# Kernel optimization log

Hardware: AMD Instinct MI355X
Metric: run time of the kernel (lower is better)

Reference implementation:

```python
import jax, jax.numpy as jnp
import numpy as np

N_E = 1024
E_DIM = 64
BETA = 0.25
DECAY = 0.99
EPSILON = 1e-5


def setup_inputs() -> dict:
    key = jax.random.key(0)
    k1, k2, k3 = jax.random.split(key, 3)
    z = jax.random.normal(k1, (32, E_DIM, 32, 32), dtype=jnp.float32)
    # codebook initialized uniform(-1/n_e, 1/n_e) as in the torch module
    emb_w = jax.random.uniform(k2, (N_E, E_DIM), minval=-1.0 / N_E, maxval=1.0 / N_E, dtype=jnp.float32)
    ema_cluster_size = jnp.ones((N_E,), dtype=jnp.float32)
    ema_w = jax.random.uniform(k3, (N_E, E_DIM), minval=-1.0 / N_E, maxval=1.0 / N_E, dtype=jnp.float32)
    return {"z": z, "emb_w": emb_w, "ema_cluster_size": ema_cluster_size, "ema_w": ema_w}


def reference(z, emb_w, ema_cluster_size, ema_w):
    B, C, H, W = z.shape  # C == E_DIM
    zf = jnp.transpose(z, (0, 2, 3, 1)).reshape(-1, E_DIM)  # [N, e_dim]
    N = zf.shape[0]

    # squared-distance via ||z||^2 + ||e||^2 - 2 z.e (same expansion as torch code)
    d = (jnp.sum(zf * zf, axis=1, keepdims=True)
         + jnp.sum(emb_w * emb_w, axis=1)
         - 2.0 * zf @ emb_w.T)  # [N, n_e]
    idx = jnp.argmin(d, axis=1)  # [N]

    min_encodings = jax.nn.one_hot(idx, N_E, dtype=jnp.float32)  # [N, n_e]
    # cluster stats via scatter-add (equivalent to one-hot matmuls, cheaper)
    cluster_size = jax.ops.segment_sum(jnp.ones((N,), jnp.float32), idx, num_segments=N_E)
    sum_encodings = jax.ops.segment_sum(zf, idx, num_segments=N_E)  # [n_e, e_dim]

    # EMA update (training path, done before the z_q lookup as in torch)
    new_cs = DECAY * ema_cluster_size + (1.0 - DECAY) * cluster_size
    new_w = DECAY * ema_w + (1.0 - DECAY) * sum_encodings
    n = jnp.sum(new_cs)
    cs_norm = (new_cs + EPSILON) / (n + N_E * EPSILON) * n
    new_emb = new_w / cs_norm[:, None]  # updated codebook

    z_q = new_emb[idx].reshape(B, H, W, C).transpose(0, 3, 1, 2)  # [B,C,H,W]
    loss = BETA * jnp.mean((jax.lax.stop_gradient(z_q) - z) ** 2)
    z_q_st = z + jax.lax.stop_gradient(z_q - z)  # straight-through

    avg_probs = cluster_size / N
    perplexity = jnp.exp(-jnp.sum(avg_probs * jnp.log(avg_probs + 1e-10)))
    return loss, z_q_st, perplexity, min_encodings, idx
```

## Files before the change

### kernel.cpp

```cpp
#include <hip/hip_runtime.h>
#include <math.h>

#define NVEC 32768
#define NE   1024
#define ED   64
#define TOT  2097152
#define NCHUNK 8
#define CHUNK  128
#define MT     64

#define O_LOSS   0
#define O_ZQ     1
#define O_PERP   2097153
#define O_MINENC 2097154
#define O_IDX    35651586

#define W_PDIST  0
#define W_PIDX   262144
#define W_CS     524288
#define W_SUMENC 525312
#define W_NEWEMB 590848
#define W_LOSSP  656384

__global__ void __launch_bounds__(256, 3) k_dist(const float* __restrict__ z,
                                                 const float* __restrict__ emb,
                                                 float* __restrict__ pdist,
                                                 int* __restrict__ pidx) {
    __shared__ __align__(16) float s_a[64 * 64];
    __shared__ __align__(16) float s_b[64 * 132];
    __shared__ float s_esq[CHUNK];
    __shared__ float s_zsq[MT];

    int tid = threadIdx.x;
    int k0 = blockIdx.y * CHUNK;
    int n0 = blockIdx.x * MT;
    int b = n0 >> 10, hw0 = n0 & 1023;
    const float* zb = z + b * 65536 + hw0;

#pragma unroll
    for (int j = 0; j < 4; ++j) {
        int f4i = j * 256 + tid;
        int c = f4i >> 4, pos = (f4i & 15) * 4;
        float4 v = *(const float4*)(zb + (c << 10) + pos);
        v.x = __fmul_rn(2.0f, v.x);
        v.y = __fmul_rn(2.0f, v.y);
        v.z = __fmul_rn(2.0f, v.z);
        v.w = __fmul_rn(2.0f, v.w);
        *(float4*)(s_a + c * 64 + pos) = v;
    }
#pragma unroll
    for (int j = 0; j < 8; ++j) {
        int f4i = j * 256 + tid;
        int kl = f4i >> 4, c0 = (f4i & 15) * 4;
        float4 v = *(const float4*)(emb + (size_t)(k0 + kl) * ED + c0);
        s_b[(c0 + 0) * 132 + kl] = v.x;
        s_b[(c0 + 1) * 132 + kl] = v.y;
        s_b[(c0 + 2) * 132 + kl] = v.z;
        s_b[(c0 + 3) * 132 + kl] = v.w;
    }
    __syncthreads();

    if (tid < 128) {
        float r[8];
#pragma unroll
        for (int j = 0; j < 8; ++j) {
            float v = s_b[j * 132 + tid];
            r[j] = __fmul_rn(v, v);
        }
#pragma unroll
        for (int i = 8; i < 64; i += 8)
#pragma unroll
            for (int j = 0; j < 8; ++j) {
                float v = s_b[(i + j) * 132 + tid];
                r[j] = __fadd_rn(r[j], __fmul_rn(v, v));
            }
        s_esq[tid] = __fadd_rn(
            __fadd_rn(__fadd_rn(r[0], r[1]), __fadd_rn(r[2], r[3])),
            __fadd_rn(__fadd_rn(r[4], r[5]), __fadd_rn(r[6], r[7])));
    } else if (tid < 192) {
        int m = tid - 128;
        float r[8];
#pragma unroll
        for (int j = 0; j < 8; ++j) {
            float v = s_a[j * 64 + m];
            r[j] = __fmul_rn(v, v);
        }
#pragma unroll
        for (int i = 8; i < 64; i += 8)
#pragma unroll
            for (int j = 0; j < 8; ++j) {
                float v = s_a[(i + j) * 64 + m];
                r[j] = __fadd_rn(r[j], __fmul_rn(v, v));
            }
        s_zsq[m] = __fmul_rn(0.25f, __fadd_rn(
            __fadd_rn(__fadd_rn(r[0], r[1]), __fadd_rn(r[2], r[3])),
            __fadd_rn(__fadd_rn(r[4], r[5]), __fadd_rn(r[6], r[7]))));
    }
    __syncthreads();

    int mi = tid & 15, ki = tid >> 4;
    int mbase = mi * 4, kbase = ki * 8;

    float acc[4][8];
#pragma unroll
    for (int mu = 0; mu < 4; ++mu)
#pragma unroll
        for (int ku = 0; ku < 8; ++ku) acc[mu][ku] = 0.f;

#pragma unroll 4
    for (int c = 0; c < 64; ++c) {
        float4 av = *(const float4*)(s_a + c * 64 + mbase);
        float4 b0 = *(const float4*)(s_b + c * 132 + kbase);
        float4 b1 = *(const float4*)(s_b + c * 132 + kbase + 4);
        const float* bv = &b0.x;
#pragma unroll
        for (int mu = 0; mu < 4; ++mu) {
            float a = (&av.x)[mu];
            acc[mu][0] = __fmaf_rn(a, b0.x, acc[mu][0]);
            acc[mu][1] = __fmaf_rn(a, b0.y, acc[mu][1]);
            acc[mu][2] = __fmaf_rn(a, b0.z, acc[mu][2]);
            acc[mu][3] = __fmaf_rn(a, b0.w, acc[mu][3]);
            acc[mu][4] = __fmaf_rn(a, b1.x, acc[mu][4]);
            acc[mu][5] = __fmaf_rn(a, b1.y, acc[mu][5]);
            acc[mu][6] = __fmaf_rn(a, b1.z, acc[mu][6]);
            acc[mu][7] = __fmaf_rn(a, b1.w, acc[mu][7]);
        }
        (void)bv;
    }

    float zs[4], es[8];
#pragma unroll
    for (int mu = 0; mu < 4; ++mu) zs[mu] = s_zsq[mbase + mu];
#pragma unroll
    for (int ku = 0; ku < 8; ++ku) es[ku] = s_esq[kbase + ku];

    float bd[4];
    int bix[4];
#pragma unroll
    for (int mu = 0; mu < 4; ++mu) {
        float best = 3.4e38f;
        int bi = k0 + kbase;
#pragma unroll
        for (int ku = 0; ku < 8; ++ku) {
            float d = __fsub_rn(__fadd_rn(zs[mu], es[ku]), acc[mu][ku]);
            if (d < best) { best = d; bi = k0 + kbase + ku; }
        }
        bd[mu] = best;
        bix[mu] = bi;
    }

    __syncthreads();
    float* red_d = s_a;
    int* red_i = (int*)(s_a + 1024);
#pragma unroll
    for (int mu = 0; mu < 4; ++mu) {
        red_d[ki * 64 + mbase + mu] = bd[mu];
        red_i[ki * 64 + mbase + mu] = bix[mu];
    }
    __syncthreads();
    if (tid < MT) {
        float best = red_d[tid];
        int bi = red_i[tid];
#pragma unroll
        for (int q = 1; q < 16; ++q) {
            float d = red_d[q * 64 + tid];
            int i = red_i[q * 64 + tid];
            if (d < best) { best = d; bi = i; }
        }
        pdist[blockIdx.y * NVEC + n0 + tid] = best;
        pidx[blockIdx.y * NVEC + n0 + tid] = bi;
    }
}

__global__ void __launch_bounds__(256) k_combine(const float* __restrict__ pdist,
                                                 int* __restrict__ pidx,
                                                 float* __restrict__ out) {
    __shared__ int sbi[64];
    int n0 = blockIdx.x * 64;
    if (threadIdx.x < 64) {
        int n = n0 + threadIdx.x;
        float best = pdist[n];
        int bi = pidx[n];
#pragma unroll
        for (int q = 1; q < NCHUNK; ++q) {
            float d = pdist[q * NVEC + n];
            int i = pidx[q * NVEC + n];
            if (d < best) { best = d; bi = i; }
        }
        pidx[n] = bi;
        out[O_IDX + n] = (float)bi;
        sbi[threadIdx.x] = bi;
    }
    __syncthreads();
    int wave = threadIdx.x >> 6, lane = threadIdx.x & 63;
    size_t base = (size_t)O_MINENC + (size_t)n0 * NE;
    for (int r = wave; r < 64; r += 4) {
        int rbi = sbi[r];
        float* rp = out + base + (size_t)r * NE;
#pragma unroll
        for (int s = 0; s < 8; ++s) {
            int col = s * 128 + lane * 2;
            float2 v;
            v.x = (col == rbi) ? 1.0f : 0.0f;
            v.y = (col + 1 == rbi) ? 1.0f : 0.0f;
            *(float2*)(rp + col) = v;
        }
    }
}

__global__ void __launch_bounds__(256) k_sumenc(const int* __restrict__ idx,
                                                const float* __restrict__ z,
                                                float* __restrict__ cs,
                                                float* __restrict__ sumenc) {
    int k = blockIdx.x;
    int wave = threadIdx.x >> 6, lane = threadIdx.x & 63;
    float acc = 0.f;
    int cnt = 0;
    int base = wave * 8192;
    for (int it = 0; it < 128; ++it) {
        int n0 = base + it * 64;
        int idv = idx[n0 + lane];
        unsigned long long m = __ballot(idv == k);
        cnt += __popcll(m);
        while (m) {
            int bit = __ffsll((unsigned long long)m) - 1;
            m &= m - 1;
            int n = n0 + bit;
            int b = n >> 10, hw = n & 1023;
            acc = __fadd_rn(acc, z[b * 65536 + lane * 1024 + hw]);
        }
    }
    __shared__ float sacc[4][64];
    __shared__ int scnt[4];
    sacc[wave][lane] = acc;
    if (lane == 0) scnt[wave] = cnt;
    __syncthreads();
    if (wave == 0) {
        float t = __fadd_rn(__fadd_rn(sacc[0][lane], sacc[1][lane]),
                            __fadd_rn(sacc[2][lane], sacc[3][lane]));
        sumenc[k * ED + lane] = t;
        if (lane == 0) cs[k] = (float)(scnt[0] + scnt[1] + scnt[2] + scnt[3]);
    }
}

__global__ void __launch_bounds__(1024) k_ema(const float* __restrict__ ema_cs,
                                              const float* __restrict__ ema_w,
                                              const float* __restrict__ cs,
                                              const float* __restrict__ sumenc,
                                              float* __restrict__ newemb,
                                              float* __restrict__ out) {
    int k = threadIdx.x;
    float c = cs[k];
    float ncs = 0.99f * ema_cs[k] + (1.0f - 0.99f) * c;
    float p = c * (1.0f / (float)NVEC);
    float e = p * logf(p + 1e-10f);
    float rn_ = ncs, re_ = e;
#pragma unroll
    for (int o = 32; o > 0; o >>= 1) {
        rn_ += __shfl_down(rn_, o, 64);
        re_ += __shfl_down(re_, o, 64);
    }
    __shared__ float sn[16], se_[16];
    __shared__ float s_n;
    int wave = k >> 6, lane = k & 63;
    if (lane == 0) { sn[wave] = rn_; se_[wave] = re_; }
    __syncthreads();
    if (k == 0) {
        float tn = 0.f, te = 0.f;
#pragma unroll
        for (int w = 0; w < 16; ++w) { tn += sn[w]; te += se_[w]; }
        s_n = tn;
        out[O_PERP] = expf(-te);
    }
    __syncthreads();
    float nt = s_n;
    float csn = (ncs + 1e-5f) / (nt + 1024.0f * 1e-5f) * nt;
    __shared__ float s_csn[NE];
    s_csn[k] = csn;
    __syncthreads();
    for (int t = k; t < NE * ED; t += 1024) {
        float nw = 0.99f * ema_w[t] + (1.0f - 0.99f) * sumenc[t];
        newemb[t] = nw / s_csn[t >> 6];
    }
}

__global__ void __launch_bounds__(256) k_zq(const float* __restrict__ z,
                                            const int* __restrict__ idx,
                                            const float* __restrict__ newemb,
                                            float* __restrict__ out,
                                            float* __restrict__ lossp) {
    float local = 0.f;
#pragma unroll
    for (int i = 0; i < 4; ++i) {
        int t = blockIdx.x * 256 + threadIdx.x + i * 524288;
        int b = t >> 16, c = (t >> 10) & 63, hw = t & 1023;
        int n = (b << 10) | hw;
        float e = newemb[idx[n] * ED + c];
        float zv = z[t];
        float diff = e - zv;
        out[O_ZQ + t] = zv + diff;
        local = fmaf(diff, diff, local);
    }
#pragma unroll
    for (int o = 32; o > 0; o >>= 1) local += __shfl_down(local, o, 64);
    __shared__ float sp[4];
    int wave = threadIdx.x >> 6;
    if ((threadIdx.x & 63) == 0) sp[wave] = local;
    __syncthreads();
    if (threadIdx.x == 0)
        lossp[blockIdx.x] = (sp[0] + sp[1]) + (sp[2] + sp[3]);
}

__global__ void __launch_bounds__(256) k_fin(const float* __restrict__ lossp,
                                             float* __restrict__ out) {
    float v = 0.f;
#pragma unroll
    for (int i = 0; i < 8; ++i) v += lossp[i * 256 + threadIdx.x];
#pragma unroll
    for (int o = 32; o > 0; o >>= 1) v += __shfl_down(v, o, 64);
    __shared__ float sp[4];
    int wave = threadIdx.x >> 6;
    if ((threadIdx.x & 63) == 0) sp[wave] = v;
    __syncthreads();
    if (threadIdx.x == 0)
        out[O_LOSS] = 0.25f * (((sp[0] + sp[1]) + (sp[2] + sp[3])) * (1.0f / (float)TOT));
}

extern "C" void kernel_launch(void* const* d_in, const int* in_sizes, int n_in,
                              void* d_out, int out_size, void* d_ws, size_t ws_size,
                              hipStream_t stream) {
    const float* z      = (const float*)d_in[0];
    const float* emb    = (const float*)d_in[1];
    const float* ema_cs = (const float*)d_in[2];
    const float* ema_w  = (const float*)d_in[3];
    float* out = (float*)d_out;
    float* ws  = (float*)d_ws;

    k_dist<<<dim3(512, NCHUNK), 256, 0, stream>>>(z, emb, ws + W_PDIST,
                                                  (int*)(ws + W_PIDX));
    k_combine<<<512, 256, 0, stream>>>(ws + W_PDIST, (int*)(ws + W_PIDX), out);
    k_sumenc<<<NE, 256, 0, stream>>>((const int*)(ws + W_PIDX), z, ws + W_CS,
                                     ws + W_SUMENC);
    k_ema<<<1, 1024, 0, stream>>>(ema_cs, ema_w, ws + W_CS, ws + W_SUMENC,
                                  ws + W_NEWEMB, out);
    k_zq<<<2048, 256, 0, stream>>>(z, (const int*)(ws + W_PIDX), ws + W_NEWEMB, out,
                                   ws + W_LOSSP);
    k_fin<<<1, 256, 0, stream>>>(ws + W_LOSSP, out);
}
```

Before: 287.2 us.

## Fuse codebook chunk loop and argmin combine into single distance kernel

The distance kernel now loops over all 8 codebook chunks inside one block, keeping a running argmin in registers, and writes the final index, float index and one-hot rows directly, so the separate combine kernel is gone. This removes the partial distance/index workspace round trip and one kernel launch. The cost is that the grid drops from 4096 blocks to 512, which may leave the GPU underoccupied, and the codebook squared norms are now read straight from global memory in every chunk. The tie-breaking in the reduction also changes slightly.

```diff
diff --git a/kernel.cpp b/kernel.cpp
--- a/kernel.cpp
+++ b/kernel.cpp
@@ -15,24 +15,23 @@
 #define O_MINENC 2097154
 #define O_IDX    35651586
 
-#define W_PDIST  0
-#define W_PIDX   262144
-#define W_CS     524288
-#define W_SUMENC 525312
-#define W_NEWEMB 590848
-#define W_LOSSP  656384
+#define W_PIDX   0
+#define W_CS     32768
+#define W_SUMENC 33792
+#define W_NEWEMB 99328
+#define W_LOSSP  164864
 
 __global__ void __launch_bounds__(256, 3) k_dist(const float* __restrict__ z,
                                                  const float* __restrict__ emb,
-                                                 float* __restrict__ pdist,
-                                                 int* __restrict__ pidx) {
+                                                 int* __restrict__ fidx,
+                                                 float* __restrict__ out) {
     __shared__ __align__(16) float s_a[64 * 64];
     __shared__ __align__(16) float s_b[64 * 132];
     __shared__ float s_esq[CHUNK];
     __shared__ float s_zsq[MT];
+    __shared__ int sbi[MT];
 
     int tid = threadIdx.x;
-    int k0 = blockIdx.y * CHUNK;
     int n0 = blockIdx.x * MT;
     int b = n0 >> 10, hw0 = n0 & 1023;
     const float* zb = z + b * 65536 + hw0;
@@ -48,51 +47,23 @@
         v.w = __fmul_rn(2.0f, v.w);
         *(float4*)(s_a + c * 64 + pos) = v;
     }
-#pragma unroll
-    for (int j = 0; j < 8; ++j) {
-        int f4i = j * 256 + tid;
-        int kl = f4i >> 4, c0 = (f4i & 15) * 4;
-        float4 v = *(const float4*)(emb + (size_t)(k0 + kl) * ED + c0);
-        s_b[(c0 + 0) * 132 + kl] = v.x;
-        s_b[(c0 + 1) * 132 + kl] = v.y;
-        s_b[(c0 + 2) * 132 + kl] = v.z;
-        s_b[(c0 + 3) * 132 + kl] = v.w;
-    }
-    __syncthreads();
-
-    if (tid < 128) {
+    __syncthreads();
+
+    if (tid < MT) {
         float r[8];
 #pragma unroll
         for (int j = 0; j < 8; ++j) {
-            float v = s_b[j * 132 + tid];
+            float v = s_a[j * 64 + tid];
             r[j] = __fmul_rn(v, v);
         }
 #pragma unroll
         for (int i = 8; i < 64; i += 8)
 #pragma unroll
             for (int j = 0; j < 8; ++j) {
-                float v = s_b[(i + j) * 132 + tid];
+                float v = s_a[(i + j) * 64 + tid];
                 r[j] = __fadd_rn(r[j], __fmul_rn(v, v));
             }
-        s_esq[tid] = __fadd_rn(
-            __fadd_rn(__fadd_rn(r[0], r[1]), __fadd_rn(r[2], r[3])),
-            __fadd_rn(__fadd_rn(r[4], r[5]), __fadd_rn(r[6], r[7])));
-    } else if (tid < 192) {
-        int m = tid - 128;
-        float r[8];
-#pragma unroll
-        for (int j = 0; j < 8; ++j) {
-            float v = s_a[j * 64 + m];
-            r[j] = __fmul_rn(v, v);
-        }
-#pragma unroll
-        for (int i = 8; i < 64; i += 8)
-#pragma unroll
-            for (int j = 0; j < 8; ++j) {
-                float v = s_a[(i + j) * 64 + m];
-                r[j] = __fadd_rn(r[j], __fmul_rn(v, v));
-            }
-        s_zsq[m] = __fmul_rn(0.25f, __fadd_rn(
+        s_zsq[tid] = __fmul_rn(0.25f, __fadd_rn(
             __fadd_rn(__fadd_rn(r[0], r[1]), __fadd_rn(r[2], r[3])),
             __fadd_rn(__fadd_rn(r[4], r[5]), __fadd_rn(r[6], r[7]))));
     }
@@ -100,58 +71,82 @@
 
     int mi = tid & 15, ki = tid >> 4;
     int mbase = mi * 4, kbase = ki * 8;
-
-    float acc[4][8];
-#pragma unroll
-    for (int mu = 0; mu < 4; ++mu)
-#pragma unroll
-        for (int ku = 0; ku < 8; ++ku) acc[mu][ku] = 0.f;
-
-#pragma unroll 4
-    for (int c = 0; c < 64; ++c) {
-        float4 av = *(const float4*)(s_a + c * 64 + mbase);
-        float4 b0 = *(const float4*)(s_b + c * 132 + kbase);
-        float4 b1 = *(const float4*)(s_b + c * 132 + kbase + 4);
-        const float* bv = &b0.x;
-#pragma unroll
-        for (int mu = 0; mu < 4; ++mu) {
-            float a = (&av.x)[mu];
-            acc[mu][0] = __fmaf_rn(a, b0.x, acc[mu][0]);
-            acc[mu][1] = __fmaf_rn(a, b0.y, acc[mu][1]);
-            acc[mu][2] = __fmaf_rn(a, b0.z, acc[mu][2]);
-            acc[mu][3] = __fmaf_rn(a, b0.w, acc[mu][3]);
-            acc[mu][4] = __fmaf_rn(a, b1.x, acc[mu][4]);
-            acc[mu][5] = __fmaf_rn(a, b1.y, acc[mu][5]);
-            acc[mu][6] = __fmaf_rn(a, b1.z, acc[mu][6]);
-            acc[mu][7] = __fmaf_rn(a, b1.w, acc[mu][7]);
-        }
-        (void)bv;
-    }
-
-    float zs[4], es[8];
+    float zs[4];
 #pragma unroll
     for (int mu = 0; mu < 4; ++mu) zs[mu] = s_zsq[mbase + mu];
-#pragma unroll
-    for (int ku = 0; ku < 8; ++ku) es[ku] = s_esq[kbase + ku];
 
     float bd[4];
     int bix[4];
 #pragma unroll
-    for (int mu = 0; mu < 4; ++mu) {
-        float best = 3.4e38f;
-        int bi = k0 + kbase;
-#pragma unroll
-        for (int ku = 0; ku < 8; ++ku) {
-            float d = __fsub_rn(__fadd_rn(zs[mu], es[ku]), acc[mu][ku]);
-            if (d < best) { best = d; bi = k0 + kbase + ku; }
-        }
-        bd[mu] = best;
-        bix[mu] = bi;
-    }
-
-    __syncthreads();
-    float* red_d = s_a;
-    int* red_i = (int*)(s_a + 1024);
+    for (int mu = 0; mu < 4; ++mu) { bd[mu] = 3.4e38f; bix[mu] = kbase; }
+
+    for (int q = 0; q < NCHUNK; ++q) {
+        int k0 = q * CHUNK;
+        __syncthreads();
+#pragma unroll
+        for (int j = 0; j < 8; ++j) {
+            int f4i = j * 256 + tid;
+            int kl = f4i >> 4, c0 = (f4i & 15) * 4;
+            float4 v = *(const float4*)(emb + (size_t)(k0 + kl) * ED + c0);
+            s_b[(c0 + 0) * 132 + kl] = v.x;
+            s_b[(c0 + 1) * 132 + kl] = v.y;
+            s_b[(c0 + 2) * 132 + kl] = v.z;
+            s_b[(c0 + 3) * 132 + kl] = v.w;
+        }
+        if (tid < CHUNK) {
+            const float* ep = emb + (size_t)(k0 + tid) * ED;
+            float r[8];
+#pragma unroll
+            for (int j = 0; j < 8; ++j) r[j] = __fmul_rn(ep[j], ep[j]);
+#pragma unroll
+            for (int i = 8; i < 64; i += 8)
+#pragma unroll
+                for (int j = 0; j < 8; ++j)
+                    r[j] = __fadd_rn(r[j], __fmul_rn(ep[i + j], ep[i + j]));
+            s_esq[tid] = __fadd_rn(
+                __fadd_rn(__fadd_rn(r[0], r[1]), __fadd_rn(r[2], r[3])),
+                __fadd_rn(__fadd_rn(r[4], r[5]), __fadd_rn(r[6], r[7])));
+        }
+        __syncthreads();
+
+        float acc[4][8];
+#pragma unroll
+        for (int mu = 0; mu < 4; ++mu)
+#pragma unroll
+            for (int ku = 0; ku < 8; ++ku) acc[mu][ku] = 0.f;
+
+#pragma unroll 4
+        for (int c = 0; c < 64; ++c) {
+            float4 av = *(const float4*)(s_a + c * 64 + mbase);
+            float4 b0 = *(const float4*)(s_b + c * 132 + kbase);
+            float4 b1 = *(const float4*)(s_b + c * 132 + kbase + 4);
+#pragma unroll
+            for (int mu = 0; mu < 4; ++mu) {
+                float a = (&av.x)[mu];
+                acc[mu][0] = __fmaf_rn(a, b0.x, acc[mu][0]);
+                acc[mu][1] = __fmaf_rn(a, b0.y, acc[mu][1]);
+                acc[mu][2] = __fmaf_rn(a, b0.z, acc[mu][2]);
+                acc[mu][3] = __fmaf_rn(a, b0.w, acc[mu][3]);
+                acc[mu][4] = __fmaf_rn(a, b1.x, acc[mu][4]);
+                acc[mu][5] = __fmaf_rn(a, b1.y, acc[mu][5]);
+                acc[mu][6] = __fmaf_rn(a, b1.z, acc[mu][6]);
+                acc[mu][7] = __fmaf_rn(a, b1.w, acc[mu][7]);
+            }
+        }
+
+#pragma unroll
+        for (int mu = 0; mu < 4; ++mu)
+#pragma unroll
+            for (int ku = 0; ku < 8; ++ku) {
+                float d = __fsub_rn(__fadd_rn(zs[mu], s_esq[kbase + ku]),
+                                    acc[mu][ku]);
+                if (d < bd[mu]) { bd[mu] = d; bix[mu] = k0 + kbase + ku; }
+            }
+    }
+
+    __syncthreads();
+    float* red_d = s_b;
+    int* red_i = (int*)(s_b + 1024);
 #pragma unroll
     for (int mu = 0; mu < 4; ++mu) {
         red_d[ki * 64 + mbase + mu] = bd[mu];
@@ -165,36 +160,16 @@
         for (int q = 1; q < 16; ++q) {
             float d = red_d[q * 64 + tid];
             int i = red_i[q * 64 + tid];
-            if (d < best) { best = d; bi = i; }
-        }
-        pdist[blockIdx.y * NVEC + n0 + tid] = best;
-        pidx[blockIdx.y * NVEC + n0 + tid] = bi;
-    }
-}
-
-__global__ void __launch_bounds__(256) k_combine(const float* __restrict__ pdist,
-                                                 int* __restrict__ pidx,
-                                                 float* __restrict__ out) {
-    __shared__ int sbi[64];
-    int n0 = blockIdx.x * 64;
-    if (threadIdx.x < 64) {
-        int n = n0 + threadIdx.x;
-        float best = pdist[n];
-        int bi = pidx[n];
-#pragma unroll
-        for (int q = 1; q < NCHUNK; ++q) {
-            float d = pdist[q * NVEC + n];
-            int i = pidx[q * NVEC + n];
-            if (d < best) { best = d; bi = i; }
-        }
-        pidx[n] = bi;
-        out[O_IDX + n] = (float)bi;
-        sbi[threadIdx.x] = bi;
-    }
-    __syncthreads();
-    int wave = threadIdx.x >> 6, lane = threadIdx.x & 63;
+            if (d < best || (d == best && i < bi)) { best = d; bi = i; }
+        }
+        fidx[n0 + tid] = bi;
+        out[O_IDX + n0 + tid] = (float)bi;
+        sbi[tid] = bi;
+    }
+    __syncthreads();
+    int wave = tid >> 6, lane = tid & 63;
     size_t base = (size_t)O_MINENC + (size_t)n0 * NE;
-    for (int r = wave; r < 64; r += 4) {
+    for (int r = wave; r < MT; r += 4) {
         int rbi = sbi[r];
         float* rp = out + base + (size_t)r * NE;
 #pragma unroll
@@ -336,9 +311,7 @@
     float* out = (float*)d_out;
     float* ws  = (float*)d_ws;
 
-    k_dist<<<dim3(512, NCHUNK), 256, 0, stream>>>(z, emb, ws + W_PDIST,
-                                                  (int*)(ws + W_PIDX));
-    k_combine<<<512, 256, 0, stream>>>(ws + W_PDIST, (int*)(ws + W_PIDX), out);
+    k_dist<<<512, 256, 0, stream>>>(z, emb, (int*)(ws + W_PIDX), out);
     k_sumenc<<<NE, 256, 0, stream>>>((const int*)(ws + W_PIDX), z, ws + W_CS,
                                      ws + W_SUMENC);
     k_ema<<<1, 1024, 0, stream>>>(ema_cs, ema_w, ws + W_CS, ws + W_SUMENC,
```

Result: slower. 293.5 us (+2.2%).
